# Kernel optimization log

Hardware: AMD Instinct MI355X
Metric: run time of the kernel (lower is better)

The kernel has to match this reference:

```python
import jax, jax.numpy as jnp
import numpy as np

B = 1024          # batch
IMG_IN = 4096     # raw visual feature dim
AUD_IN = 1024     # raw audio feature dim
ENC = 1024        # encoder output dim
S = 3             # multi-scale branches (768 = 3*256 in out_layer)
D = 256           # MmFA feature dim (hardcoded in module)
OUT1 = 512
LAT = 128         # minus_one_dim
NCLS = 10
NORM = 1.0 / np.sqrt(256.0)  # note: original applies this AFTER softmax


def setup_inputs() -> dict:
    key = jax.random.key(0)
    ks = jax.random.split(key, 16)
    n = lambda k, shape, s=0.02: jax.random.normal(k, shape, dtype=jnp.float32) * s
    return dict(
        img=jax.random.normal(ks[0], (B, IMG_IN), dtype=jnp.float32),
        audio=jax.random.normal(ks[1], (B, AUD_IN), dtype=jnp.float32),
        vis_W=n(ks[2], (ENC, IMG_IN)), vis_b=jnp.zeros((ENC,), jnp.float32),
        aud_W=n(ks[3], (ENC, AUD_IN)), aud_b=jnp.zeros((ENC,), jnp.float32),
        msv_W=n(ks[4], (S, D, ENC)), msv_b=jnp.zeros((S, D), jnp.float32),
        msa_W=n(ks[5], (S, D, ENC)), msa_b=jnp.zeros((S, D), jnp.float32),
        mmfa_W=n(ks[6], (8, D, D)),  # q_v,q_a,k_v,k_a,w1,w2,w3,w4
        mmfa_b=jnp.zeros((8, D), jnp.float32),
        bil_W=n(ks[7], (D, D, D)),   # nn.Bilinear(256,256,256,bias=False)
        t_c=jnp.ones((), jnp.float32),
        out_W1=n(ks[8], (OUT1, S * D)), out_b1=jnp.zeros((OUT1,), jnp.float32),
        out_W2=n(ks[9], (LAT, OUT1)), out_b2=jnp.zeros((LAT,), jnp.float32),
        clsv_W1=n(ks[10], (32, LAT)), clsv_W2=n(ks[11], (NCLS, 32)),
        clsa_W1=n(ks[12], (32, LAT)), clsa_W2=n(ks[13], (NCLS, 32)),
    )


def _mmfa(x_v, x_a, W, b, bil_W, t_c):
    # x_v, x_a: [B, S, D]
    lin = lambda i, x: jnp.einsum('bsd,kd->bsk', x, W[i]) + b[i]
    q_v, q_a, k_v, k_a = lin(0, x_v), lin(1, x_a), lin(2, x_v), lin(3, x_a)
    # faithful to source: softmax first, then scale by 1/sqrt(dim_k)
    att = lambda q, k: jax.nn.softmax(jnp.einsum('bsd,btd->bst', q, k), axis=-1) * NORM
    alpha_va = jnp.einsum('bst,btd->bsd', att(q_v, k_a), x_a)
    alpha_v = jnp.einsum('bst,btd->bsd', att(q_v, k_v), x_v)
    alpha_av = jnp.einsum('bst,btd->bsd', att(q_a, k_v), x_v)
    alpha_a = jnp.einsum('bst,btd->bsd', att(q_a, k_a), x_a)
    c_va = jax.nn.sigmoid((lin(4, alpha_va) + lin(5, alpha_v)) * alpha_v)
    c_av = jax.nn.sigmoid((lin(6, alpha_av) + lin(7, alpha_a)) * alpha_a)
    j = jax.nn.sigmoid(jnp.einsum('bsi,oij,bsj->bso', c_va, bil_W, c_av))
    return t_c * j * x_v + (1.0 - j) * x_a


def reference(img, audio, vis_W, vis_b, aud_W, aud_b, msv_W, msv_b, msa_W, msa_b,
              mmfa_W, mmfa_b, bil_W, t_c, out_W1, out_b1, out_W2, out_b2,
              clsv_W1, clsv_W2, clsa_W1, clsa_W2):
    vis = jax.nn.relu(img @ vis_W.T + vis_b)       # [B, ENC]
    aud = jax.nn.relu(audio @ aud_W.T + aud_b)     # [B, ENC]
    # reconstructed MultiScale_Modal_Net: 3 parallel Linear(ENC->D)+ReLU -> [B,S,D]
    v_ms = jax.nn.relu(jnp.einsum('bd,skd->bsk', vis, msv_W) + msv_b)
    a_ms = jax.nn.relu(jnp.einsum('bd,skd->bsk', aud, msa_W) + msa_b)
    M1 = _mmfa(v_ms, a_ms, mmfa_W, mmfa_b, bil_W, t_c)
    M2 = _mmfa(M1 * v_ms, M1 * a_ms, mmfa_W, mmfa_b, bil_W, t_c)
    ov = (M2 * v_ms).reshape(img.shape[0], -1)     # [B, 768]
    oa = (M2 * a_ms).reshape(img.shape[0], -1)
    # out_layer (dropout = identity in eval)
    fv = jax.nn.relu(ov @ out_W1.T + out_b1) @ out_W2.T + out_b2   # [B, 128]
    fa = jax.nn.relu(oa @ out_W1.T + out_b1) @ out_W2.T + out_b2
    pv = jax.nn.relu(fv @ clsv_W1.T) @ clsv_W2.T                   # [B, 10]
    pa = jax.nn.relu(fa @ clsa_W1.T) @ clsa_W2.T
    return (fv, fa, pv, pa)
```

## Files before the change

kernel.cpp:

```cpp
#include <hip/hip_runtime.h>
#include <math.h>


typedef short short8   __attribute__((ext_vector_type(8)));
typedef float floatx4  __attribute__((ext_vector_type(4)));

constexpr float NORM = 0.0625f;

__device__ __forceinline__ unsigned short f2bf(float f) {
    union { float f; unsigned int u; } v; v.f = f;
    unsigned int r = v.u + 0x7fffu + ((v.u >> 16) & 1u);
    return (unsigned short)(r >> 16);
}
__device__ __forceinline__ float bf2f(unsigned short s) {
    union { unsigned int u; float f; } v; v.u = ((unsigned int)s) << 16;
    return v.f;
}

template<int ACT>
__global__ __launch_bounds__(256)
void gemm_mfma_z(const float* __restrict__ A0, const float* __restrict__ A1,
                 const unsigned short* __restrict__ Wp0,
                 const unsigned short* __restrict__ Wp1,
                 const float* __restrict__ b0, const float* __restrict__ b1,
                 float* __restrict__ C0, float* __restrict__ C1,
                 int M, int N, int K)
{
    const float* A = blockIdx.z ? A1 : A0;
    const unsigned short* W = blockIdx.z ? Wp1 : Wp0;
    const float* bias = blockIdx.z ? b1 : b0;
    float* C = blockIdx.z ? C1 : C0;

    __shared__ short sA[64][72];
    __shared__ short sW[64][72];
    const int tid  = threadIdx.x;
    const int wave = tid >> 6, lane = tid & 63;
    const int quad = lane >> 4, l15 = lane & 15;
    const int m0 = blockIdx.y * 64, n0 = blockIdx.x * 64;
    const int mw = (wave & 1) * 32, nw = (wave >> 1) * 32;
    const int srow = tid >> 2, sseg = tid & 3;

    floatx4 P[2][2];
    #pragma unroll
    for (int f = 0; f < 2; f++)
        #pragma unroll
        for (int g = 0; g < 2; g++)
            P[f][g] = (floatx4){0.f, 0.f, 0.f, 0.f};

    for (int k0 = 0; k0 < K; k0 += 64) {
        const float* ap = A + (size_t)(m0 + srow) * K + k0 + sseg * 16;
        float4 a0 = *(const float4*)(ap);
        float4 a1 = *(const float4*)(ap + 4);
        float4 a2 = *(const float4*)(ap + 8);
        float4 a3 = *(const float4*)(ap + 12);
        union { unsigned short s[8]; short8 v; } p0, p1;
        p0.s[0] = f2bf(a0.x); p0.s[1] = f2bf(a0.y); p0.s[2] = f2bf(a0.z); p0.s[3] = f2bf(a0.w);
        p0.s[4] = f2bf(a1.x); p0.s[5] = f2bf(a1.y); p0.s[6] = f2bf(a1.z); p0.s[7] = f2bf(a1.w);
        p1.s[0] = f2bf(a2.x); p1.s[1] = f2bf(a2.y); p1.s[2] = f2bf(a2.z); p1.s[3] = f2bf(a2.w);
        p1.s[4] = f2bf(a3.x); p1.s[5] = f2bf(a3.y); p1.s[6] = f2bf(a3.z); p1.s[7] = f2bf(a3.w);
        *(short8*)&sA[srow][sseg * 16]     = p0.v;
        *(short8*)&sA[srow][sseg * 16 + 8] = p1.v;
        const unsigned short* wp = W + (size_t)(n0 + srow) * K + k0 + sseg * 16;
        *(short8*)&sW[srow][sseg * 16]     = *(const short8*)wp;
        *(short8*)&sW[srow][sseg * 16 + 8] = *(const short8*)(wp + 8);
        __syncthreads();
        #pragma unroll
        for (int kh = 0; kh < 2; kh++) {
            short8 af[2], wf[2];
            af[0] = *(short8*)&sA[mw + l15][kh * 32 + quad * 8];
            af[1] = *(short8*)&sA[mw + 16 + l15][kh * 32 + quad * 8];
            wf[0] = *(short8*)&sW[nw + l15][kh * 32 + quad * 8];
            wf[1] = *(short8*)&sW[nw + 16 + l15][kh * 32 + quad * 8];
            #pragma unroll
            for (int f = 0; f < 2; f++)
                #pragma unroll
                for (int g = 0; g < 2; g++)
                    P[f][g] = __builtin_amdgcn_mfma_f32_16x16x32_bf16(af[f], wf[g], P[f][g], 0, 0, 0);
        }
        __syncthreads();
    }
    #pragma unroll
    for (int f = 0; f < 2; f++)
        #pragma unroll
        for (int g = 0; g < 2; g++)
            #pragma unroll
            for (int r = 0; r < 4; r++) {
                int m = m0 + mw + 16 * f + quad * 4 + r;
                int n = n0 + nw + 16 * g + l15;
                float v = P[f][g][r] + bias[n];
                if (ACT) v = fmaxf(v, 0.f);
                C[(size_t)m * N + n] = v;
            }
}

__global__ __launch_bounds__(256)
void gemm_sigm_z(const float* __restrict__ A0, const float* __restrict__ A1,
                 const unsigned short* __restrict__ Wp0,
                 const unsigned short* __restrict__ Wp1,
                 const float* __restrict__ b0, const float* __restrict__ b1,
                 unsigned short* __restrict__ O0, unsigned short* __restrict__ O1,
                 int M, int N, int K)
{
    const float* A = blockIdx.z ? A1 : A0;
    const unsigned short* W = blockIdx.z ? Wp1 : Wp0;
    const float* bias = blockIdx.z ? b1 : b0;
    unsigned short* Cbf = blockIdx.z ? O1 : O0;

    __shared__ short sA[64][72];
    __shared__ short sW[64][72];
    const int tid  = threadIdx.x;
    const int wave = tid >> 6, lane = tid & 63;
    const int quad = lane >> 4, l15 = lane & 15;
    const int m0 = blockIdx.y * 64, n0 = blockIdx.x * 64;
    const int mw = (wave & 1) * 32, nw = (wave >> 1) * 32;
    const int srow = tid >> 2, sseg = tid & 3;

    floatx4 P[2][2];
    #pragma unroll
    for (int f = 0; f < 2; f++)
        #pragma unroll
        for (int g = 0; g < 2; g++)
            P[f][g] = (floatx4){0.f, 0.f, 0.f, 0.f};

    for (int k0 = 0; k0 < K; k0 += 64) {
        const float* ap = A + (size_t)(m0 + srow) * K + k0 + sseg * 16;
        float4 a0 = *(const float4*)(ap);
        float4 a1 = *(const float4*)(ap + 4);
        float4 a2 = *(const float4*)(ap + 8);
        float4 a3 = *(const float4*)(ap + 12);
        union { unsigned short s[8]; short8 v; } p0, p1;
        p0.s[0] = f2bf(a0.x); p0.s[1] = f2bf(a0.y); p0.s[2] = f2bf(a0.z); p0.s[3] = f2bf(a0.w);
        p0.s[4] = f2bf(a1.x); p0.s[5] = f2bf(a1.y); p0.s[6] = f2bf(a1.z); p0.s[7] = f2bf(a1.w);
        p1.s[0] = f2bf(a2.x); p1.s[1] = f2bf(a2.y); p1.s[2] = f2bf(a2.z); p1.s[3] = f2bf(a2.w);
        p1.s[4] = f2bf(a3.x); p1.s[5] = f2bf(a3.y); p1.s[6] = f2bf(a3.z); p1.s[7] = f2bf(a3.w);
        *(short8*)&sA[srow][sseg * 16]     = p0.v;
        *(short8*)&sA[srow][sseg * 16 + 8] = p1.v;
        const unsigned short* wp = W + (size_t)(n0 + srow) * K + k0 + sseg * 16;
        *(short8*)&sW[srow][sseg * 16]     = *(const short8*)wp;
        *(short8*)&sW[srow][sseg * 16 + 8] = *(const short8*)(wp + 8);
        __syncthreads();
        #pragma unroll
        for (int kh = 0; kh < 2; kh++) {
            short8 af[2], wf[2];
            af[0] = *(short8*)&sA[mw + l15][kh * 32 + quad * 8];
            af[1] = *(short8*)&sA[mw + 16 + l15][kh * 32 + quad * 8];
            wf[0] = *(short8*)&sW[nw + l15][kh * 32 + quad * 8];
            wf[1] = *(short8*)&sW[nw + 16 + l15][kh * 32 + quad * 8];
            #pragma unroll
            for (int f = 0; f < 2; f++)
                #pragma unroll
                for (int g = 0; g < 2; g++)
                    P[f][g] = __builtin_amdgcn_mfma_f32_16x16x32_bf16(af[f], wf[g], P[f][g], 0, 0, 0);
        }
        __syncthreads();
    }
    #pragma unroll
    for (int f = 0; f < 2; f++)
        #pragma unroll
        for (int g = 0; g < 2; g++)
            #pragma unroll
            for (int r = 0; r < 4; r++) {
                int m = m0 + mw + 16 * f + quad * 4 + r;
                int n = n0 + nw + 16 * g + l15;
                float v = P[f][g][r] + bias[n];
                float a = A[(size_t)m * 512 + 256 + n];
                Cbf[(size_t)m * N + n] = f2bf(1.f / (1.f + expf(-v * a)));
            }
}

__global__ __launch_bounds__(256)
void conv_multi(const float* __restrict__ s0, unsigned short* __restrict__ d0,
                const float* __restrict__ s1, unsigned short* __restrict__ d1,
                const float* __restrict__ s2, unsigned short* __restrict__ d2,
                const float* __restrict__ s3, unsigned short* __restrict__ d3,
                const float* __restrict__ s4, unsigned short* __restrict__ d4,
                const float* __restrict__ s5, unsigned short* __restrict__ d5)
{
    long long g = ((long long)blockIdx.x * 256 + threadIdx.x) * 8;
    const float* src; unsigned short* dst; long long off = g;
    if      (off < 4194304)                 { src = s0; dst = d0; }
    else if ((off = g - 4194304) < 1048576) { src = s1; dst = d1; }
    else if ((off = g - 5242880) < 786432)  { src = s2; dst = d2; }
    else if ((off = g - 6029312) < 786432)  { src = s3; dst = d3; }
    else if ((off = g - 6815744) < 393216)  { src = s4; dst = d4; }
    else if ((off = g - 7208960) < 65536)   { src = s5; dst = d5; }
    else return;
    float4 a = *(const float4*)(src + off);
    float4 b = *(const float4*)(src + off + 4);
    union { unsigned short s[8]; uint4 v; } o;
    o.s[0] = f2bf(a.x); o.s[1] = f2bf(a.y); o.s[2] = f2bf(a.z); o.s[3] = f2bf(a.w);
    o.s[4] = f2bf(b.x); o.s[5] = f2bf(b.y); o.s[6] = f2bf(b.z); o.s[7] = f2bf(b.w);
    *(uint4*)(dst + off) = o.v;
}

__global__ __launch_bounds__(256)
void pack_mmfa(const float* __restrict__ mW, const float* __restrict__ mb,
               unsigned short* __restrict__ Wqkv, unsigned short* __restrict__ Wqka,
               unsigned short* __restrict__ Wcva, unsigned short* __restrict__ Wcav,
               float* __restrict__ bqkv, float* __restrict__ bqka,
               float* __restrict__ bcva, float* __restrict__ bcav)
{
    int b = blockIdx.x;
    if (b < 2048) {
        int i = b * 256 + threadIdx.x;
        int w = i >> 16, r = i & 65535;
        unsigned short s = f2bf(mW[i]);
        int row = r >> 8, col = r & 255;
        switch (w) {
            case 0: Wqkv[r] = s; break;
            case 1: Wqka[r] = s; break;
            case 2: Wqkv[65536 + r] = s; break;
            case 3: Wqka[65536 + r] = s; break;
            case 4: Wcva[row * 512 + col] = s; break;
            case 5: Wcva[row * 512 + 256 + col] = s; break;
            case 6: Wcav[row * 512 + col] = s; break;
            case 7: Wcav[row * 512 + 256 + col] = s; break;
        }
    } else {
        int i = threadIdx.x;
        for (int t = i; t < 512; t += 256) {
            int c = t & 255;
            bqkv[t] = mb[(t < 256 ? 0 : 512) + c];
            bqka[t] = mb[(t < 256 ? 256 : 768) + c];
        }
        bcva[i] = mb[1024 + i] + mb[1280 + i];
        bcav[i] = mb[1536 + i] + mb[1792 + i];
    }
}

__global__ __launch_bounds__(512, 4)
void bilinear_col(const unsigned short* __restrict__ cav,
                  const unsigned short* __restrict__ cva,
                  const float* __restrict__ Wf,
                  float* __restrict__ outT)
{
    __shared__ short sA[64][264];
    __shared__ float sRed[8][64];
    const int tid  = threadIdx.x;
    const int wave = tid >> 6, lane = tid & 63;
    const int quad = lane >> 4, l15 = lane & 15;
    const int o     = blockIdx.x;
    const int mbase = blockIdx.y * 768;
    const int i0    = wave * 32;

    short8 Wr[2][8];
    {
        const float* wo = Wf + (size_t)o * 65536;
        #pragma unroll
        for (int f = 0; f < 2; f++) {
            const float* wrow = wo + (size_t)(i0 + 16 * f + l15) * 256 + quad * 8;
            #pragma unroll
            for (int s = 0; s < 8; s++) {
                float4 lo = *(const float4*)(wrow + s * 32);
                float4 hi = *(const float4*)(wrow + s * 32 + 4);
                union { unsigned short u[8]; short8 v; } p;
                p.u[0] = f2bf(lo.x); p.u[1] = f2bf(lo.y); p.u[2] = f2bf(lo.z); p.u[3] = f2bf(lo.w);
                p.u[4] = f2bf(hi.x); p.u[5] = f2bf(hi.y); p.u[6] = f2bf(hi.z); p.u[7] = f2bf(hi.w);
                Wr[f][s] = p.v;
            }
        }
    }

    const int srow = tid >> 3, sseg = tid & 7;
    for (int ms = 0; ms < 12; ms++) {
        const int m0 = mbase + ms * 64;
        __syncthreads();
        {
            const unsigned short* src = cav + (size_t)(m0 + srow) * 256 + sseg * 32;
            #pragma unroll
            for (int u = 0; u < 4; u++)
                *(short8*)&sA[srow][sseg * 32 + u * 8] = *(const short8*)(src + u * 8);
        }
        __syncthreads();

        uint2 raws[2][4];
        #pragma unroll
        for (int g = 0; g < 4; g++)
            #pragma unroll
            for (int f = 0; f < 2; f++)
                raws[f][g] = *(const uint2*)(cva + (size_t)(m0 + 16 * g + l15) * 256
                                                  + i0 + 16 * f + 4 * quad);

        floatx4 P2[2][4];
        #pragma unroll
        for (int f = 0; f < 2; f++)
            #pragma unroll
            for (int g = 0; g < 4; g++)
                P2[f][g] = (floatx4){0.f, 0.f, 0.f, 0.f};

        #pragma unroll
        for (int s = 0; s < 8; s++) {
            short8 bg[4];
            #pragma unroll
            for (int g = 0; g < 4; g++)
                bg[g] = *(const short8*)&sA[16 * g + l15][s * 32 + quad * 8];
            #pragma unroll
            for (int f = 0; f < 2; f++)
                #pragma unroll
                for (int g = 0; g < 4; g++)
                    P2[f][g] = __builtin_amdgcn_mfma_f32_16x16x32_bf16(Wr[f][s], bg[g], P2[f][g], 0, 0, 0);
        }

        float T[4] = {0.f, 0.f, 0.f, 0.f};
        #pragma unroll
        for (int g = 0; g < 4; g++)
            #pragma unroll
            for (int f = 0; f < 2; f++) {
                uint2 raw = raws[f][g];
                T[g] += bf2f((unsigned short)(raw.x & 0xffff)) * P2[f][g][0]
                      + bf2f((unsigned short)(raw.x >> 16))    * P2[f][g][1]
                      + bf2f((unsigned short)(raw.y & 0xffff)) * P2[f][g][2]
                      + bf2f((unsigned short)(raw.y >> 16))    * P2[f][g][3];
            }
        #pragma unroll
        for (int g = 0; g < 4; g++) {
            T[g] += __shfl_xor(T[g], 16);
            T[g] += __shfl_xor(T[g], 32);
        }
        if (quad == 0) {
            #pragma unroll
            for (int g = 0; g < 4; g++)
                sRed[wave][16 * g + l15] = T[g];
        }
        __syncthreads();
        if (tid < 64) {
            float acc = sRed[0][tid] + sRed[1][tid] + sRed[2][tid] + sRed[3][tid]
                      + sRed[4][tid] + sRed[5][tid] + sRed[6][tid] + sRed[7][tid];
            outT[(size_t)o * 3072 + m0 + tid] = acc;
        }
    }
}

__global__ __launch_bounds__(256)
void attn_packed(const float* __restrict__ qkv, const float* __restrict__ qka,
                 const float* __restrict__ xv, const float* __restrict__ xa,
                 float* __restrict__ al_v, float* __restrict__ al_a)
{
    const int b    = blockIdx.x;
    const int tid  = threadIdx.x;
    const int wave = tid >> 6;
    const int lane = tid & 63;
    __shared__ float att[4][3][3];
    const size_t b512 = (size_t)b * 1536;
    const size_t b768 = (size_t)b * 768;
    const float* Qs[4] = {qkv, qkv, qka, qka};
    const float* Ks[4] = {qka + 256, qkv + 256, qkv + 256, qka + 256};
    const float* Xs[4] = {xa, xv, xv, xa};
    float*       Os[4] = {al_v, al_v + 256, al_a, al_a + 256};
    const float* q = Qs[wave] + b512;
    const float* k = Ks[wave] + b512;
    float part[9] = {};
    for (int d = lane; d < 256; d += 64) {
        float q0 = q[d], q1 = q[512 + d], q2 = q[1024 + d];
        float k0 = k[d], k1 = k[512 + d], k2 = k[1024 + d];
        part[0] += q0 * k0; part[1] += q0 * k1; part[2] += q0 * k2;
        part[3] += q1 * k0; part[4] += q1 * k1; part[5] += q1 * k2;
        part[6] += q2 * k0; part[7] += q2 * k1; part[8] += q2 * k2;
    }
    #pragma unroll
    for (int off = 32; off > 0; off >>= 1)
        #pragma unroll
        for (int i = 0; i < 9; i++) part[i] += __shfl_down(part[i], off);
    if (lane == 0) {
        #pragma unroll
        for (int s = 0; s < 3; s++) {
            float a0 = part[s * 3], a1 = part[s * 3 + 1], a2 = part[s * 3 + 2];
            float mx = fmaxf(a0, fmaxf(a1, a2));
            float e0 = expf(a0 - mx), e1 = expf(a1 - mx), e2 = expf(a2 - mx);
            float inv = NORM / (e0 + e1 + e2);
            att[wave][s][0] = e0 * inv;
            att[wave][s][1] = e1 * inv;
            att[wave][s][2] = e2 * inv;
        }
    }
    __syncthreads();
    const int d = tid;
    #pragma unroll
    for (int w = 0; w < 4; w++) {
        const float* x = Xs[w] + b768;
        float x0 = x[d], x1 = x[256 + d], x2 = x[512 + d];
        float* o = Os[w] + b512;
        #pragma unroll
        for (int s = 0; s < 3; s++)
            o[s * 512 + d] = att[w][s][0] * x0 + att[w][s][1] * x1 + att[w][s][2] * x2;
    }
}

__global__ void ew_mix(const float* __restrict__ logitsT, const float* __restrict__ xv,
                       const float* __restrict__ xa, const float* __restrict__ bv,
                       const float* __restrict__ ba, const float* __restrict__ tc,
                       float* __restrict__ outv, float* __restrict__ outa, int n)
{
    int i = blockIdx.x * 256 + threadIdx.x;
    if (i < n) {
        int m = i >> 8, o = i & 255;
        float j = 1.f / (1.f + expf(-logitsT[(size_t)o * 3072 + m]));
        float M = tc[0] * j * xv[i] + (1.f - j) * xa[i];
        outv[i] = M * bv[i];
        outa[i] = M * ba[i];
    }
}

__global__ __launch_bounds__(256)
void cls_fused(const float* __restrict__ fv, const float* __restrict__ fa,
               const float* __restrict__ Wv1, const float* __restrict__ Wv2,
               const float* __restrict__ Wa1, const float* __restrict__ Wa2,
               float* __restrict__ pv, float* __restrict__ pa)
{
    const int z = blockIdx.y;
    const float* F  = z ? fa  : fv;
    const float* W1 = z ? Wa1 : Wv1;
    const float* W2 = z ? Wa2 : Wv2;
    float* Pp       = z ? pa  : pv;
    __shared__ float sX[64][132];
    __shared__ float sW1[32][133];
    __shared__ float sH[64][33];
    __shared__ float sW2[320];
    const int tid = threadIdx.x;
    const int r0  = blockIdx.x * 64;
    for (int u = tid; u < 64 * 32; u += 256) {
        int row = u >> 5, seg = u & 31;
        *(float4*)&sX[row][seg * 4] = *(const float4*)(F + (size_t)(r0 + row) * 128 + seg * 4);
    }
    for (int u = tid; u < 32 * 128; u += 256) {
        int row = u >> 7, k = u & 127;
        sW1[row][k] = W1[row * 128 + k];
    }
    if (tid < 80) ((float4*)sW2)[tid] = ((const float4*)W2)[tid];
    __syncthreads();
    const int r = tid >> 2, jg = (tid & 3) * 8;
    float h[8] = {};
    for (int k = 0; k < 128; k++) {
        float x = sX[r][k];
        #pragma unroll
        for (int j = 0; j < 8; j++) h[j] += x * sW1[jg + j][k];
    }
    #pragma unroll
    for (int j = 0; j < 8; j++) sH[r][jg + j] = fmaxf(h[j], 0.f);
    __syncthreads();
    for (int u = tid; u < 640; u += 256) {
        int row = u / 10, oo = u % 10;
        float acc = 0.f;
        #pragma unroll
        for (int j = 0; j < 32; j++) acc += sH[row][j] * sW2[oo * 32 + j];
        Pp[(size_t)(r0 + row) * 10 + oo] = acc;
    }
}

extern "C" void kernel_launch(void* const* d_in, const int* in_sizes, int n_in,
                              void* d_out, int out_size, void* d_ws, size_t ws_size,
                              hipStream_t stream)
{
    const float* img    = (const float*)d_in[0];
    const float* audio  = (const float*)d_in[1];
    const float* vis_W  = (const float*)d_in[2];
    const float* vis_b  = (const float*)d_in[3];
    const float* aud_W  = (const float*)d_in[4];
    const float* aud_b  = (const float*)d_in[5];
    const float* msv_W  = (const float*)d_in[6];
    const float* msv_b  = (const float*)d_in[7];
    const float* msa_W  = (const float*)d_in[8];
    const float* msa_b  = (const float*)d_in[9];
    const float* mmfa_W = (const float*)d_in[10];
    const float* mmfa_b = (const float*)d_in[11];
    const float* bil_W  = (const float*)d_in[12];
    const float* t_c    = (const float*)d_in[13];
    const float* out_W1 = (const float*)d_in[14];
    const float* out_b1 = (const float*)d_in[15];
    const float* out_W2 = (const float*)d_in[16];
    const float* out_b2 = (const float*)d_in[17];
    const float* clsv_W1 = (const float*)d_in[18];
    const float* clsv_W2 = (const float*)d_in[19];
    const float* clsa_W1 = (const float*)d_in[20];
    const float* clsa_W2 = (const float*)d_in[21];
    float* out = (float*)d_out;
    float* ws  = (float*)d_ws;

    constexpr size_t SD = 3072 * 256;
    float* S = ws;
    unsigned short* visbf = (unsigned short*)(S + 2097152);
    unsigned short* audbf = (unsigned short*)(S + 4194304);
    unsigned short* msvbf = (unsigned short*)(S + 4718592);
    unsigned short* msabf = (unsigned short*)(S + 5111808);
    float* vis  = S;
    float* aud  = S + 1048576;
    float* qkv  = S;
    float* qka  = S + 1572864;
    float* al_v = S + 3145728;
    float* al_a = S + 4718592;
    float* ovb  = S;
    float* oab  = S + SD;
    float* hv1  = S + 2 * SD;
    float* hv2  = S + 2 * SD + 524288;
    float* P = ws + 8388608;
    float* v_ms    = P;
    float* a_ms    = P + SD;
    float* x_v2    = P + 2 * SD;
    float* x_a2    = P + 3 * SD;
    float* logitsT = P + 4 * SD;
    unsigned short* c_va = (unsigned short*)(P + 5 * SD);
    unsigned short* c_av = (unsigned short*)(P + 5 * SD + SD / 2);
    unsigned short* Wqkv = (unsigned short*)(P + 6 * SD);
    unsigned short* Wqka = Wqkv + 131072;
    unsigned short* Wcva = Wqka + 131072;
    unsigned short* Wcav = Wcva + 131072;
    float* bqkv = P + 6 * SD + 262144;
    float* bqka = bqkv + 512;
    float* bcva = bqka + 512;
    float* bcav = bcva + 256;
    unsigned short* W1bf = (unsigned short*)(bcav + 256);
    unsigned short* W2bf = W1bf + 393216;

    conv_multi<<<3552, 256, 0, stream>>>(vis_W, visbf, aud_W, audbf,
                                         msv_W, msvbf, msa_W, msabf,
                                         out_W1, W1bf, out_W2, W2bf);
    pack_mmfa<<<2049, 256, 0, stream>>>(mmfa_W, mmfa_b, Wqkv, Wqka, Wcva, Wcav,
                                        bqkv, bqka, bcva, bcav);

    gemm_mfma_z<1><<<dim3(16, 16, 1), 256, 0, stream>>>(
        img, img, visbf, visbf, vis_b, vis_b, vis, vis, 1024, 1024, 4096);
    gemm_mfma_z<1><<<dim3(16, 16, 1), 256, 0, stream>>>(
        audio, audio, audbf, audbf, aud_b, aud_b, aud, aud, 1024, 1024, 1024);
    gemm_mfma_z<1><<<dim3(12, 16, 2), 256, 0, stream>>>(
        vis, aud, msvbf, msabf, msv_b, msa_b, v_ms, a_ms, 1024, 768, 1024);

    const int EW_N = (int)SD;
    const int EW_G = (EW_N + 255) / 256;

    auto mmfa = [&](const float* xv, const float* xa, float* outv, float* outa) {
        gemm_mfma_z<0><<<dim3(8, 48, 2), 256, 0, stream>>>(
            xv, xa, Wqkv, Wqka, bqkv, bqka, qkv, qka, 3072, 512, 256);
        attn_packed<<<1024, 256, 0, stream>>>(qkv, qka, xv, xa, al_v, al_a);
        gemm_sigm_z<<<dim3(4, 48, 2), 256, 0, stream>>>(
            al_v, al_a, Wcva, Wcav, bcva, bcav, c_va, c_av, 3072, 256, 512);
        bilinear_col<<<dim3(256, 4), 512, 0, stream>>>(c_av, c_va, bil_W, logitsT);
        ew_mix<<<EW_G, 256, 0, stream>>>(logitsT, xv, xa, v_ms, a_ms, t_c,
                                         outv, outa, EW_N);
    };

    mmfa(v_ms, a_ms, x_v2, x_a2);
    mmfa(x_v2, x_a2, ovb, oab);

    float* fv = out;
    float* fa = out + 1024 * 128;
    float* pv = out + 2 * 1024 * 128;
    float* pa = pv + 1024 * 10;

    gemm_mfma_z<1><<<dim3(8, 16, 2), 256, 0, stream>>>(
        ovb, oab, W1bf, W1bf, out_b1, out_b1, hv1, hv2, 1024, 512, 768);
    gemm_mfma_z<0><<<dim3(2, 16, 2), 256, 0, stream>>>(
        hv1, hv2, W2bf, W2bf, out_b2, out_b2, fv, fa, 1024, 128, 512);
    cls_fused<<<dim3(16, 2), 256, 0, stream>>>(fv, fa, clsv_W1, clsv_W2,
                                               clsa_W1, clsa_W2, pv, pa);

    (void)in_sizes; (void)n_in; (void)out_size; (void)ws_size;
}
```

Measured before the change: 781.3 us.

## Double-buffer bilinear reductions, halve its grid, and tile-transpose the mix kernel

The bilinear kernel now covers 1536 rows per block over 24 sub-tiles, so each block converts its weight slice to bf16 once for twice as many rows and the grid shrinks from 4 to 2 along M. The cross-wave reduction buffer is double-buffered, and the previous tile's reduction and store are folded into the next iteration, which removes one __syncthreads per tile. The elementwise mix kernel is rewritten to stage 64x64 tiles of the transposed logits in shared memory, giving coalesced reads and float4 accesses instead of strided logit gathers. The trade-off is fewer bilinear blocks (512 instead of 1024), which lowers parallelism and occupancy on the GPU.

```diff
diff --git a/kernel.cpp b/kernel.cpp
--- a/kernel.cpp
+++ b/kernel.cpp
@@ -235,12 +235,12 @@
                   float* __restrict__ outT)
 {
     __shared__ short sA[64][264];
-    __shared__ float sRed[8][64];
+    __shared__ float sRed[2][8][64];
     const int tid  = threadIdx.x;
     const int wave = tid >> 6, lane = tid & 63;
     const int quad = lane >> 4, l15 = lane & 15;
     const int o     = blockIdx.x;
-    const int mbase = blockIdx.y * 768;
+    const int mbase = blockIdx.y * 1536;
     const int i0    = wave * 32;
 
     short8 Wr[2][8];
@@ -262,7 +262,7 @@
     }
 
     const int srow = tid >> 3, sseg = tid & 7;
-    for (int ms = 0; ms < 12; ms++) {
+    for (int ms = 0; ms < 24; ms++) {
         const int m0 = mbase + ms * 64;
         __syncthreads();
         {
@@ -270,6 +270,13 @@
             #pragma unroll
             for (int u = 0; u < 4; u++)
                 *(short8*)&sA[srow][sseg * 32 + u * 8] = *(const short8*)(src + u * 8);
+        }
+        if (ms > 0 && tid < 64) {
+            const int pb = (ms - 1) & 1;
+            float acc = sRed[pb][0][tid] + sRed[pb][1][tid] + sRed[pb][2][tid]
+                      + sRed[pb][3][tid] + sRed[pb][4][tid] + sRed[pb][5][tid]
+                      + sRed[pb][6][tid] + sRed[pb][7][tid];
+            outT[(size_t)o * 3072 + m0 - 64 + tid] = acc;
         }
         __syncthreads();
 
@@ -320,14 +327,15 @@
         if (quad == 0) {
             #pragma unroll
             for (int g = 0; g < 4; g++)
-                sRed[wave][16 * g + l15] = T[g];
-        }
-        __syncthreads();
-        if (tid < 64) {
-            float acc = sRed[0][tid] + sRed[1][tid] + sRed[2][tid] + sRed[3][tid]
-                      + sRed[4][tid] + sRed[5][tid] + sRed[6][tid] + sRed[7][tid];
-            outT[(size_t)o * 3072 + m0 + tid] = acc;
-        }
+                sRed[ms & 1][wave][16 * g + l15] = T[g];
+        }
+    }
+    __syncthreads();
+    if (tid < 64) {
+        float acc = sRed[1][0][tid] + sRed[1][1][tid] + sRed[1][2][tid]
+                  + sRed[1][3][tid] + sRed[1][4][tid] + sRed[1][5][tid]
+                  + sRed[1][6][tid] + sRed[1][7][tid];
+        outT[(size_t)o * 3072 + mbase + 23 * 64 + tid] = acc;
     }
 }
 
@@ -386,18 +394,45 @@
     }
 }
 
-__global__ void ew_mix(const float* __restrict__ logitsT, const float* __restrict__ xv,
-                       const float* __restrict__ xa, const float* __restrict__ bv,
-                       const float* __restrict__ ba, const float* __restrict__ tc,
-                       float* __restrict__ outv, float* __restrict__ outa, int n)
-{
-    int i = blockIdx.x * 256 + threadIdx.x;
-    if (i < n) {
-        int m = i >> 8, o = i & 255;
-        float j = 1.f / (1.f + expf(-logitsT[(size_t)o * 3072 + m]));
-        float M = tc[0] * j * xv[i] + (1.f - j) * xa[i];
-        outv[i] = M * bv[i];
-        outa[i] = M * ba[i];
+__global__ __launch_bounds__(256)
+void ew_mix_t(const float* __restrict__ logitsT, const float* __restrict__ xv,
+              const float* __restrict__ xa, const float* __restrict__ bv,
+              const float* __restrict__ ba, const float* __restrict__ tc,
+              float* __restrict__ outv, float* __restrict__ outa)
+{
+    __shared__ float sL[64][65];
+    const int tid = threadIdx.x;
+    const int m0 = blockIdx.x * 64, o0 = blockIdx.y * 64;
+    {
+        int r = tid >> 2, cs = (tid & 3) * 16;
+        const float* src = logitsT + (size_t)(o0 + r) * 3072 + m0 + cs;
+        #pragma unroll
+        for (int u = 0; u < 4; u++)
+            *(float4*)&sL[r][cs + u * 4] = *(const float4*)(src + u * 4);
+    }
+    __syncthreads();
+    const float tcv = tc[0];
+    int mr = tid >> 2, os = (tid & 3) * 16;
+    size_t base = (size_t)(m0 + mr) * 256 + o0 + os;
+    #pragma unroll
+    for (int u = 0; u < 4; u++) {
+        float4 xvv = *(const float4*)(xv + base + u * 4);
+        float4 xav = *(const float4*)(xa + base + u * 4);
+        float4 bvv = *(const float4*)(bv + base + u * 4);
+        float4 bav = *(const float4*)(ba + base + u * 4);
+        float4 ov, oa;
+        float* pxv = (float*)&xvv; float* pxa = (float*)&xav;
+        float* pbv = (float*)&bvv; float* pba = (float*)&bav;
+        float* pov = (float*)&ov;  float* poa = (float*)&oa;
+        #pragma unroll
+        for (int e = 0; e < 4; e++) {
+            float j = 1.f / (1.f + expf(-sL[os + u * 4 + e][mr]));
+            float M = tcv * j * pxv[e] + (1.f - j) * pxa[e];
+            pov[e] = M * pbv[e];
+            poa[e] = M * pba[e];
+        }
+        *(float4*)(outv + base + u * 4) = ov;
+        *(float4*)(outa + base + u * 4) = oa;
     }
 }
 
@@ -524,18 +559,15 @@
     gemm_mfma_z<1><<<dim3(12, 16, 2), 256, 0, stream>>>(
         vis, aud, msvbf, msabf, msv_b, msa_b, v_ms, a_ms, 1024, 768, 1024);
 
-    const int EW_N = (int)SD;
-    const int EW_G = (EW_N + 255) / 256;
-
     auto mmfa = [&](const float* xv, const float* xa, float* outv, float* outa) {
         gemm_mfma_z<0><<<dim3(8, 48, 2), 256, 0, stream>>>(
             xv, xa, Wqkv, Wqka, bqkv, bqka, qkv, qka, 3072, 512, 256);
         attn_packed<<<1024, 256, 0, stream>>>(qkv, qka, xv, xa, al_v, al_a);
         gemm_sigm_z<<<dim3(4, 48, 2), 256, 0, stream>>>(
             al_v, al_a, Wcva, Wcav, bcva, bcav, c_va, c_av, 3072, 256, 512);
-        bilinear_col<<<dim3(256, 4), 512, 0, stream>>>(c_av, c_va, bil_W, logitsT);
-        ew_mix<<<EW_G, 256, 0, stream>>>(logitsT, xv, xa, v_ms, a_ms, t_c,
-                                         outv, outa, EW_N);
+        bilinear_col<<<dim3(256, 2), 512, 0, stream>>>(c_av, c_va, bil_W, logitsT);
+        ew_mix_t<<<dim3(48, 4), 256, 0, stream>>>(logitsT, xv, xa, v_ms, a_ms,
+                                                  t_c, outv, outa);
     };
 
     mmfa(v_ms, a_ms, x_v2, x_a2);
```

Result: faster. 731.2 us (-6.4%).
